# Performance work log

Hardware: AMD Instinct MI355X
Metric: run time of the kernel (lower is better)

## Reference

```python
import jax, jax.numpy as jnp
import numpy as np

SCALE = 8      # scale_factor from map_to_mat_info
PATCH = 32     # up_delta - low_delta + 1 == right_delta - left_delta + 1 (uniform interior patches)


def setup_inputs() -> dict:
    key = jax.random.key(0)
    mat_h, mat_w = 160, 160
    H = (mat_h - 1) * SCALE + PATCH  # 1304: deltas (0,31,0,31) -> no border clipping
    W = (mat_w - 1) * SCALE + PATCH
    x = jax.random.normal(key, (1, 3, H, W), dtype=jnp.float32)
    rgb_weight = jnp.array([0.299, 0.587, 0.114], dtype=jnp.float32).reshape(1, 3, 1, 1)
    return {"x": x, "rgb_weight": rgb_weight, "mat_h": mat_h, "mat_w": mat_w}


def reference(x, rgb_weight, mat_h, mat_w):
    P = PATCH
    # RGB -> grayscale (convert_gray branch for in_channels == 3)
    gray = jnp.sum(x * rgb_weight, axis=1)[0]  # (H, W)
    # Gather all overlapping PxP patches at stride SCALE -> (mat_h, mat_w, P, P)
    rows = (jnp.arange(mat_h) * SCALE)[:, None] + jnp.arange(P)[None, :]  # (mat_h, P)
    cols = (jnp.arange(mat_w) * SCALE)[:, None] + jnp.arange(P)[None, :]  # (mat_w, P)
    p = gray[rows.reshape(-1)].reshape(mat_h, P, -1)              # (mat_h, P, W)
    p = p[:, :, cols.reshape(-1)].reshape(mat_h, P, mat_w, P)     # (mat_h, P, mat_w, P)
    patches = jnp.transpose(p, (0, 2, 1, 3))                      # (mat_h, mat_w, P, P)
    # torch.rfft(signal_ndim=2, onesided=False) == full 2D FFT; power = re^2 + im^2
    F = jnp.fft.fft2(patches)
    log_power = jnp.log(F.real * F.real + F.imag * F.imag + 1.0)
    # High-frequency region sums (h == w == P, static)
    lo = P // 2 - P // 4 - 1   # 7
    up = P // 2 + P // 4       # 24
    r1 = jnp.sum(log_power[..., lo:up + 1, :], axis=(-2, -1))
    r2 = jnp.sum(log_power[..., up + 1:, lo:up + 1], axis=(-2, -1))
    r3 = jnp.sum(log_power[..., :lo, lo:up + 1], axis=(-2, -1))
    mat = (r1 + r2 + r3)[None, None]  # (1, 1, mat_h, mat_w)
    return mat / jnp.max(mat)
```

## Files before the change

kernel.cpp:

```cpp
#include <hip/hip_runtime.h>
#include <math.h>

#define SCALE 8
#define PSZ 32

__device__ constexpr float C32[16] = {
     1.000000000000000f,  0.980785280403230f,  0.923879532511287f,  0.831469612302545f,
     0.707106781186548f,  0.555570233019602f,  0.382683432365090f,  0.195090322016128f,
     0.000000000000000f, -0.195090322016128f, -0.382683432365090f, -0.555570233019602f,
    -0.707106781186548f, -0.831469612302545f, -0.923879532511287f, -0.980785280403230f };
__device__ constexpr float S32[16] = {
     0.000000000000000f,  0.195090322016128f,  0.382683432365090f,  0.555570233019602f,
     0.707106781186548f,  0.831469612302545f,  0.923879532511287f,  0.980785280403230f,
     1.000000000000000f,  0.980785280403230f,  0.923879532511287f,  0.831469612302545f,
     0.707106781186548f,  0.555570233019602f,  0.382683432365090f,  0.195090322016128f };

__device__ __forceinline__ constexpr int brev5(int i) {
    return ((i & 1) << 4) | ((i & 2) << 2) | (i & 4) | ((i & 8) >> 2) | ((i & 16) >> 4);
}

__device__ __forceinline__ void fft32(float re[PSZ], float im[PSZ]) {
#pragma unroll
    for (int i = 0; i < 32; ++i) {
        const int j = brev5(i);
        if (j > i) {
            float t = re[i]; re[i] = re[j]; re[j] = t;
            t = im[i]; im[i] = im[j]; im[j] = t;
        }
    }
#pragma unroll
    for (int s = 1; s <= 5; ++s) {
        const int m = 1 << s;
        const int h = m >> 1;
        const int tstep = 32 >> s;
#pragma unroll
        for (int k = 0; k < 32; k += m) {
#pragma unroll
            for (int j = 0; j < h; ++j) {
                const float wr = C32[j * tstep];
                const float wi = -S32[j * tstep];
                const int a = k + j;
                const int b = k + j + h;
                const float tr = wr * re[b] - wi * im[b];
                const float ti = wr * im[b] + wi * re[b];
                re[b] = re[a] - tr; im[b] = im[a] - ti;
                re[a] = re[a] + tr; im[a] = im[a] + ti;
            }
        }
    }
}

__device__ __forceinline__ unsigned pack_bf2(float hi, float lo) {
    const unsigned uh = __float_as_uint(hi) + 0x8000u;
    const unsigned ul = __float_as_uint(lo) + 0x8000u;
    return (uh & 0xFFFF0000u) | (ul >> 16);
}
__device__ __forceinline__ float bf_hi(unsigned u) { return __uint_as_float(u & 0xFFFF0000u); }
__device__ __forceinline__ float bf_lo(unsigned u) { return __uint_as_float(u << 16); }

__global__ __launch_bounds__(64) void hfdft_patch_kernel(
        const float* __restrict__ x, const float* __restrict__ w,
        float* __restrict__ out, int H, int W, int mat_h, int mat_w) {
    __shared__ unsigned cb[4 * 528];

    const int lane = threadIdx.x;
    const int total = mat_h * mat_w;
    const float w0 = w[0], w1 = w[1], w2 = w[2];
    const long long HW = (long long)H * W;

    {
        const int g = lane >> 5, r = lane & 31;
        int pA = blockIdx.x * 4 + 2 * g;
        if (pA > total - 1) pA = total - 1;
        int pB = pA + 1; if (pB > total - 1) pB = total - 1;
        const int phA = pA / mat_w, pwA = pA % mat_w;
        const int phB = pB / mat_w, pwB = pB % mat_w;
        const bool adj = (phA == phB) && (pwB == pwA + 1);

        float re[PSZ], im[PSZ];
        if (adj && ((W & 3) == 0)) {
            const int base = (phA * SCALE + r) * W + pwA * SCALE;
            const float4* a4 = reinterpret_cast<const float4*>(x + base);
            const float4* b4 = reinterpret_cast<const float4*>(x + HW + base);
            const float4* c4 = reinterpret_cast<const float4*>(x + 2 * HW + base);
            float win[40];
#pragma unroll
            for (int q = 0; q < 10; ++q) {
                const float4 a = a4[q], b = b4[q], c = c4[q];
                win[4 * q + 0] = w0 * a.x + w1 * b.x + w2 * c.x;
                win[4 * q + 1] = w0 * a.y + w1 * b.y + w2 * c.y;
                win[4 * q + 2] = w0 * a.z + w1 * b.z + w2 * c.z;
                win[4 * q + 3] = w0 * a.w + w1 * b.w + w2 * c.w;
            }
#pragma unroll
            for (int i = 0; i < PSZ; ++i) { re[i] = win[i]; im[i] = win[i + 8]; }
        } else {
            const int baseA = (phA * SCALE + r) * W + pwA * SCALE;
            const int baseB = (phB * SCALE + r) * W + pwB * SCALE;
#pragma unroll
            for (int i = 0; i < PSZ; ++i) {
                re[i] = w0 * x[baseA + i] + w1 * x[HW + baseA + i] + w2 * x[2 * HW + baseA + i];
                im[i] = w0 * x[baseB + i] + w1 * x[HW + baseB + i] + w2 * x[2 * HW + baseB + i];
            }
        }

        fft32(re, im);

        unsigned* cbA = cb + (2 * g) * 528;
        unsigned* cbB = cb + (2 * g + 1) * 528;
        cbA[r] = pack_bf2(re[0], re[16]);
        cbB[r] = pack_bf2(im[0], im[16]);
#pragma unroll
        for (int k = 1; k <= 15; ++k) {
            const int m = 32 - k;
            const float far_ = 0.5f * (re[k] + re[m]);
            const float fai_ = 0.5f * (im[k] - im[m]);
            const float fbr_ = 0.5f * (im[k] + im[m]);
            const float fbi_ = 0.5f * (re[m] - re[k]);
            cbA[k * 33 + r] = pack_bf2(far_, fai_);
            cbB[k * 33 + r] = pack_bf2(fbr_, fbi_);
        }
    }

    __syncthreads();

    {
        const int pl = lane >> 4, slot = lane & 15;
        const int p = blockIdx.x * 4 + pl;
        const unsigned* cbp = cb + pl * 528 + slot * 33;

        float cre[PSZ], cim[PSZ];
#pragma unroll
        for (int r2 = 0; r2 < PSZ; ++r2) {
            const unsigned u = cbp[r2];
            cre[r2] = bf_hi(u);
            cim[r2] = bf_lo(u);
        }

        fft32(cre, cim);

        float s = 0.0f;
        if (slot == 0) {
#pragma unroll
            for (int kr = 0; kr <= 16; ++kr) {
                const int m = (32 - kr) & 31;
                const float g0r = 0.5f * (cre[kr] + cre[m]);
                const float g0i = 0.5f * (cim[kr] - cim[m]);
                const float g1r = 0.5f * (cim[kr] + cim[m]);
                const float g1i = 0.5f * (cre[m] - cre[kr]);
                const float w0c = (kr >= 7 ? 1.0f : 0.0f) + ((kr >= 8 && kr <= 15) ? 1.0f : 0.0f);
                const float w16c = 1.0f + ((kr >= 1 && kr <= 15) ? 1.0f : 0.0f);
                if (w0c > 0.0f)
                    s = fmaf(w0c, __logf(g0r * g0r + g0i * g0i + 1.0f), s);
                s = fmaf(w16c, __logf(g1r * g1r + g1i * g1i + 1.0f), s);
            }
        } else {
            const float b1f = (slot >= 7) ? 1.0f : 0.0f;
            const float m1f = (slot >= 8) ? 1.0f : 0.0f;
#pragma unroll
            for (int kr = 0; kr < 32; ++kr) {
                const float lp = __logf(cre[kr] * cre[kr] + cim[kr] * cim[kr] + 1.0f);
                float wgt;
                if (kr >= 8 && kr <= 24)      wgt = 2.0f;
                else if (kr == 7)             wgt = 1.0f + m1f;
                else if (kr == 25)            wgt = b1f + 1.0f;
                else                          wgt = b1f + m1f;
                if (!(kr >= 8 && kr <= 24))   s = fmaf(wgt, lp, s);
                else                          s = fmaf(2.0f, lp, s);
            }
        }

#pragma unroll
        for (int off = 8; off >= 1; off >>= 1) s += __shfl_xor(s, off, 16);
        if (slot == 0 && p < total) out[p] = s;
    }
}

__global__ __launch_bounds__(1024) void max_kernel(
        const float* __restrict__ sums, int n, float* __restrict__ mx) {
    __shared__ float sm[16];
    float m = 0.0f;
    for (int i = threadIdx.x; i < n; i += 1024) m = fmaxf(m, sums[i]);
#pragma unroll
    for (int off = 32; off >= 1; off >>= 1) m = fmaxf(m, __shfl_xor(m, off, 64));
    if ((threadIdx.x & 63) == 0) sm[threadIdx.x >> 6] = m;
    __syncthreads();
    if (threadIdx.x == 0) {
#pragma unroll
        for (int i = 1; i < 16; ++i) m = fmaxf(m, sm[i]);
        mx[0] = m;
    }
}

__global__ __launch_bounds__(256) void norm_kernel(
        float* __restrict__ out, int n, const float* __restrict__ mx) {
    const int i = blockIdx.x * 256 + threadIdx.x;
    if (i < n) out[i] = out[i] / mx[0];
}

extern "C" void kernel_launch(void* const* d_in, const int* in_sizes, int n_in,
                              void* d_out, int out_size, void* d_ws, size_t ws_size,
                              hipStream_t stream) {
    const float* x = (const float*)d_in[0];
    const float* w = (const float*)d_in[1];
    float* out = (float*)d_out;
    float* maxbuf = (float*)d_ws;

    const int HW = in_sizes[0] / 3;
    const int H = (int)(sqrt((double)HW) + 0.5);
    const int W = H;
    const int mat = (int)(sqrt((double)out_size) + 0.5);
    const int total = mat * mat;

    const int blocksA = (total + 3) / 4;
    hipLaunchKernelGGL(hfdft_patch_kernel, dim3(blocksA), dim3(64), 0, stream,
                       x, w, out, H, W, mat, mat);
    hipLaunchKernelGGL(max_kernel, dim3(1), dim3(1024), 0, stream, out, total, maxbuf);
    hipLaunchKernelGGL(norm_kernel, dim3((total + 255) / 256), dim3(256), 0, stream,
                       out, total, maxbuf);
}
```

Measured before the change: 44.12 us.

## Fuse max reduction via atomicMax, swizzle LDS layout, two waves per block

Drops the single-block max kernel and computes the global max with an atomicMax on the float bits (valid because every sum is non-negative), seeded by a memset. The shared-memory stride-33 padding is replaced by an XOR swizzle. Each block now runs two waves covering eight patches instead of one wave covering four. The log-sum accumulation is split into two independent accumulators for more instruction-level parallelism. This removes a serial one-block launch, at the cost of an extra memset and many atomics landing on one address.

```diff
diff --git a/kernel.cpp b/kernel.cpp
--- a/kernel.cpp
+++ b/kernel.cpp
@@ -58,19 +58,23 @@
 __device__ __forceinline__ float bf_hi(unsigned u) { return __uint_as_float(u & 0xFFFF0000u); }
 __device__ __forceinline__ float bf_lo(unsigned u) { return __uint_as_float(u << 16); }
 
-__global__ __launch_bounds__(64) void hfdft_patch_kernel(
+__global__ __launch_bounds__(128) void hfdft_patch_kernel(
         const float* __restrict__ x, const float* __restrict__ w,
-        float* __restrict__ out, int H, int W, int mat_h, int mat_w) {
-    __shared__ unsigned cb[4 * 528];
-
-    const int lane = threadIdx.x;
+        float* __restrict__ out, unsigned* __restrict__ mx,
+        int H, int W, int mat_h, int mat_w) {
+    __shared__ unsigned cb[8 * 512];
+
+    const int tid = threadIdx.x;
+    const int wid = tid >> 6;
+    const int lane = tid & 63;
+    const int P0 = blockIdx.x * 8 + wid * 4;
     const int total = mat_h * mat_w;
     const float w0 = w[0], w1 = w[1], w2 = w[2];
     const long long HW = (long long)H * W;
 
     {
         const int g = lane >> 5, r = lane & 31;
-        int pA = blockIdx.x * 4 + 2 * g;
+        int pA = P0 + 2 * g;
         if (pA > total - 1) pA = total - 1;
         int pB = pA + 1; if (pB > total - 1) pB = total - 1;
         const int phA = pA / mat_w, pwA = pA % mat_w;
@@ -106,8 +110,8 @@
 
         fft32(re, im);
 
-        unsigned* cbA = cb + (2 * g) * 528;
-        unsigned* cbB = cb + (2 * g + 1) * 528;
+        unsigned* cbA = cb + (wid * 4 + 2 * g) * 512;
+        unsigned* cbB = cbA + 512;
         cbA[r] = pack_bf2(re[0], re[16]);
         cbB[r] = pack_bf2(im[0], im[16]);
 #pragma unroll
@@ -117,8 +121,9 @@
             const float fai_ = 0.5f * (im[k] - im[m]);
             const float fbr_ = 0.5f * (im[k] + im[m]);
             const float fbi_ = 0.5f * (re[m] - re[k]);
-            cbA[k * 33 + r] = pack_bf2(far_, fai_);
-            cbB[k * 33 + r] = pack_bf2(fbr_, fbi_);
+            const int idx = (k << 5) + (r ^ (2 * k));
+            cbA[idx] = pack_bf2(far_, fai_);
+            cbB[idx] = pack_bf2(fbr_, fbi_);
         }
     }
 
@@ -126,20 +131,21 @@
 
     {
         const int pl = lane >> 4, slot = lane & 15;
-        const int p = blockIdx.x * 4 + pl;
-        const unsigned* cbp = cb + pl * 528 + slot * 33;
+        const int p = P0 + pl;
+        const unsigned* cbp = cb + (wid * 4 + pl) * 512 + (slot << 5);
+        const int s2 = 2 * slot;
 
         float cre[PSZ], cim[PSZ];
 #pragma unroll
         for (int r2 = 0; r2 < PSZ; ++r2) {
-            const unsigned u = cbp[r2];
+            const unsigned u = cbp[r2 ^ s2];
             cre[r2] = bf_hi(u);
             cim[r2] = bf_lo(u);
         }
 
         fft32(cre, cim);
 
-        float s = 0.0f;
+        float s0 = 0.0f, s1 = 0.0f;
         if (slot == 0) {
 #pragma unroll
             for (int kr = 0; kr <= 16; ++kr) {
@@ -151,8 +157,8 @@
                 const float w0c = (kr >= 7 ? 1.0f : 0.0f) + ((kr >= 8 && kr <= 15) ? 1.0f : 0.0f);
                 const float w16c = 1.0f + ((kr >= 1 && kr <= 15) ? 1.0f : 0.0f);
                 if (w0c > 0.0f)
-                    s = fmaf(w0c, __logf(g0r * g0r + g0i * g0i + 1.0f), s);
-                s = fmaf(w16c, __logf(g1r * g1r + g1i * g1i + 1.0f), s);
+                    s0 = fmaf(w0c, __logf(g0r * g0r + g0i * g0i + 1.0f), s0);
+                s1 = fmaf(w16c, __logf(g1r * g1r + g1i * g1i + 1.0f), s1);
             }
         } else {
             const float b1f = (slot >= 7) ? 1.0f : 0.0f;
@@ -165,37 +171,25 @@
                 else if (kr == 7)             wgt = 1.0f + m1f;
                 else if (kr == 25)            wgt = b1f + 1.0f;
                 else                          wgt = b1f + m1f;
-                if (!(kr >= 8 && kr <= 24))   s = fmaf(wgt, lp, s);
-                else                          s = fmaf(2.0f, lp, s);
-            }
-        }
+                if (kr & 1) s1 = fmaf(wgt, lp, s1);
+                else        s0 = fmaf(wgt, lp, s0);
+            }
+        }
+        float s = s0 + s1;
 
 #pragma unroll
         for (int off = 8; off >= 1; off >>= 1) s += __shfl_xor(s, off, 16);
-        if (slot == 0 && p < total) out[p] = s;
-    }
-}
-
-__global__ __launch_bounds__(1024) void max_kernel(
-        const float* __restrict__ sums, int n, float* __restrict__ mx) {
-    __shared__ float sm[16];
-    float m = 0.0f;
-    for (int i = threadIdx.x; i < n; i += 1024) m = fmaxf(m, sums[i]);
-#pragma unroll
-    for (int off = 32; off >= 1; off >>= 1) m = fmaxf(m, __shfl_xor(m, off, 64));
-    if ((threadIdx.x & 63) == 0) sm[threadIdx.x >> 6] = m;
-    __syncthreads();
-    if (threadIdx.x == 0) {
-#pragma unroll
-        for (int i = 1; i < 16; ++i) m = fmaxf(m, sm[i]);
-        mx[0] = m;
+        if (slot == 0 && p < total) {
+            out[p] = s;
+            atomicMax(mx, __float_as_uint(s));
+        }
     }
 }
 
 __global__ __launch_bounds__(256) void norm_kernel(
-        float* __restrict__ out, int n, const float* __restrict__ mx) {
+        float* __restrict__ out, int n, const unsigned* __restrict__ mx) {
     const int i = blockIdx.x * 256 + threadIdx.x;
-    if (i < n) out[i] = out[i] / mx[0];
+    if (i < n) out[i] = out[i] / __uint_as_float(mx[0]);
 }
 
 extern "C" void kernel_launch(void* const* d_in, const int* in_sizes, int n_in,
@@ -204,7 +198,7 @@
     const float* x = (const float*)d_in[0];
     const float* w = (const float*)d_in[1];
     float* out = (float*)d_out;
-    float* maxbuf = (float*)d_ws;
+    unsigned* maxbuf = (unsigned*)d_ws;
 
     const int HW = in_sizes[0] / 3;
     const int H = (int)(sqrt((double)HW) + 0.5);
@@ -212,10 +206,11 @@
     const int mat = (int)(sqrt((double)out_size) + 0.5);
     const int total = mat * mat;
 
-    const int blocksA = (total + 3) / 4;
-    hipLaunchKernelGGL(hfdft_patch_kernel, dim3(blocksA), dim3(64), 0, stream,
-                       x, w, out, H, W, mat, mat);
-    hipLaunchKernelGGL(max_kernel, dim3(1), dim3(1024), 0, stream, out, total, maxbuf);
+    hipMemsetAsync(maxbuf, 0, 4, stream);
+
+    const int blocksA = (total + 7) / 8;
+    hipLaunchKernelGGL(hfdft_patch_kernel, dim3(blocksA), dim3(128), 0, stream,
+                       x, w, out, maxbuf, H, W, mat, mat);
     hipLaunchKernelGGL(norm_kernel, dim3((total + 255) / 256), dim3(256), 0, stream,
                        out, total, maxbuf);
 }
```

New measurement: 99.08 us. 2.25x slower.
